# Kernel optimization log

Measured on AMD Instinct MI355X. Metric: run time of the kernel, lower is better.

## Reference

```python
import jax, jax.numpy as jnp
import numpy as np

B, R, C, H, W = 4, 2, 19, 256, 512


def setup_inputs() -> dict:
    key = jax.random.key(0)
    k1, k2, k3 = jax.random.split(key, 3)
    return {
        "ref_pred": jax.random.normal(k1, (B, R, C, H, W), dtype=jnp.float32),
        # motion vectors in quarter-pel units (divided by 4 inside forward);
        # scale so displacements span a few pixels
        "ref_mv": jax.random.normal(k2, (B, R, 2, H, W), dtype=jnp.float32) * 8.0,
        "ref_weight": jax.random.uniform(k3, (B, R, 1, H, W), dtype=jnp.float32),
    }


def _warp(img, mv):
    """Bilinear backward warp (grid_sample, zeros padding).
    img: [N, C, H, W], mv: [N, 2, H, W] pixel displacements (x, y)."""
    N, Ch, Hh, Ww = img.shape
    ys, xs = jnp.meshgrid(jnp.arange(Hh, dtype=mv.dtype),
                          jnp.arange(Ww, dtype=mv.dtype), indexing="ij")
    gx = xs + mv[:, 0]  # [N, H, W] sample x-coordinate
    gy = ys + mv[:, 1]  # [N, H, W] sample y-coordinate
    x0 = jnp.floor(gx); y0 = jnp.floor(gy)
    x1 = x0 + 1.0;      y1 = y0 + 1.0
    wx1 = gx - x0; wx0 = 1.0 - wx1
    wy1 = gy - y0; wy0 = 1.0 - wy1

    img_flat = img.reshape(N, Ch, Hh * Ww)

    def samp(iy, ix):
        valid = ((ix >= 0) & (ix <= Ww - 1) & (iy >= 0) & (iy <= Hh - 1))
        iyc = jnp.clip(iy, 0, Hh - 1).astype(jnp.int32)
        ixc = jnp.clip(ix, 0, Ww - 1).astype(jnp.int32)
        lin = (iyc * Ww + ixc).reshape(N, 1, Hh * Ww)
        vals = jnp.take_along_axis(
            img_flat, jnp.broadcast_to(lin, (N, Ch, Hh * Ww)), axis=2
        ).reshape(N, Ch, Hh, Ww)
        return vals * valid.astype(img.dtype)[:, None]

    out = (samp(y0, x0) * (wy0 * wx0)[:, None]
           + samp(y0, x1) * (wy0 * wx1)[:, None]
           + samp(y1, x0) * (wy1 * wx0)[:, None]
           + samp(y1, x1) * (wy1 * wx1)[:, None])
    return out


def reference(ref_pred, ref_mv, ref_weight):
    Bb, Rr = ref_pred.shape[:2]
    pred = ref_pred.reshape(Bb * Rr, *ref_pred.shape[2:])   # [B*R, C, H, W]
    mv = ref_mv.reshape(Bb * Rr, *ref_mv.shape[2:]) / 4.0    # quarter-pel -> pixel
    # eval mode, eval_noise_sigma=0 -> no noise added
    warped = _warp(pred, mv)                                  # [B*R, C, H, W]
    w = ref_weight.reshape(Bb * Rr, *ref_weight.shape[2:])   # [B*R, 1, H, W]
    warped = warped * w
    return warped.reshape(Bb, Rr, *warped.shape[1:]).sum(axis=1)  # [B, C, H, W]
```

## Files before the change

### kernel.cpp

```cpp
#include <hip/hip_runtime.h>

constexpr int B = 4, R = 2, C = 19, H = 256, W = 512;
constexpr int HW = H * W;

constexpr int BX = 64, BY = 16;
constexpr int NBX = W / BX;
constexpr int NBY = H / BY;
constexpr int NSPAT = B * NBX * NBY;

constexpr int TW = 92;
constexpr int TH = 42;
constexpr int TILE_N = TW * TH;
constexpr int TILE_V4 = TILE_N / 4;

__global__ __launch_bounds__(256, 4) void mc_warp_kernel(
    const float* __restrict__ pred,
    const float* __restrict__ mv,
    const float* __restrict__ wgt,
    float* __restrict__ out)
{
    __shared__ float tile0[TILE_N];
    __shared__ float tile1[TILE_N];

    int t = threadIdx.x;
    int xcd  = blockIdx.x & 7;
    int slot = blockIdx.x >> 3;
    int vblk = xcd * (NSPAT / 8) + slot;
    int bx   = vblk & (NBX - 1);
    int by   = (vblk >> 3) & (NBY - 1);
    int b    = vblk >> 7;
    int x0 = bx * BX, y0 = by * BY;
    int tx = t & 15, ty = t >> 4;
    int y  = y0 + ty;
    int xb = x0 + tx * 4;

    int rowbase = min(max(y0 - 12, 0), H - TH);
    int colbase = min(max(x0 - 12, 0), W - TW);

    int   off0[R][4], off1[R][4];
    int   offL0[R][4], offL1[R][4], offG0[R][4], offG1[R][4];
    float wq[R][4][4];
    int flag = 0;

    #pragma unroll
    for (int r = 0; r < R; ++r) {
        const float* mvp = mv + (size_t)((b * R + r) * 2) * HW + (size_t)y * W + xb;
        float4 mx4 = *(const float4*)(mvp);
        float4 my4 = *(const float4*)(mvp + HW);
        float4 wr4 = *(const float4*)(wgt + (size_t)(b * R + r) * HW + (size_t)y * W + xb);
        float mxs[4] = {mx4.x, mx4.y, mx4.z, mx4.w};
        float mys[4] = {my4.x, my4.y, my4.z, my4.w};
        float wrs[4] = {wr4.x, wr4.y, wr4.z, wr4.w};
        #pragma unroll
        for (int p = 0; p < 4; ++p) {
            int x = xb + p;
            float gx = (float)x + mxs[p] * 0.25f;
            float gy = (float)y + mys[p] * 0.25f;
            float fx0 = floorf(gx), fy0 = floorf(gy);
            float wx1 = gx - fx0, wx0 = 1.0f - wx1;
            float wy1 = gy - fy0, wy0 = 1.0f - wy1;
            int ix0 = (int)fx0, iy0 = (int)fy0;
            int ix1 = ix0 + 1,  iy1 = iy0 + 1;

            int base = min(max(ix0, 0), W - 2);
            float wA = (ix0 == base)     ? wx0 : ((ix1 == base)     ? wx1 : 0.0f);
            float wB = (ix1 == base + 1) ? wx1 : ((ix0 == base + 1) ? wx0 : 0.0f);
            float wr = wrs[p];
            float wy0v = ((iy0 >= 0) && (iy0 < H)) ? wy0 * wr : 0.0f;
            float wy1v = ((iy1 >= 0) && (iy1 < H)) ? wy1 * wr : 0.0f;
            int cy0 = min(max(iy0, 0), H - 1);
            int cy1 = min(max(iy1, 0), H - 1);

            int l0 = base - colbase;
            int r0 = cy0 - rowbase, r1 = cy1 - rowbase;
            bool anyx = (wA != 0.0f) || (wB != 0.0f);
            bool anyy = (wy0v != 0.0f) || (wy1v != 0.0f);
            bool cb  = (l0 < 0 || l0 > TW - 2) && anyx && anyy;
            bool rb0 = (r0 < 0 || r0 > TH - 1) && (wy0v != 0.0f) && anyx;
            bool rb1 = (r1 < 0 || r1 > TH - 1) && (wy1v != 0.0f) && anyx;
            flag |= (int)(cb || rb0 || rb1);
            l0 = min(max(l0, 0), TW - 2);
            r0 = min(max(r0, 0), TH - 1);
            r1 = min(max(r1, 0), TH - 1);

            offL0[r][p] = r0 * TW + l0;
            offL1[r][p] = r1 * TW + l0;
            offG0[r][p] = cy0 * W + base;
            offG1[r][p] = cy1 * W + base;
            wq[r][p][0] = wy0v * wA;
            wq[r][p][1] = wy0v * wB;
            wq[r][p][2] = wy1v * wA;
            wq[r][p][3] = wy1v * wB;
        }
    }

    int fbB = __syncthreads_or(flag);
    #pragma unroll
    for (int r = 0; r < R; ++r)
        #pragma unroll
        for (int p = 0; p < 4; ++p) {
            off0[r][p] = fbB ? offG0[r][p] : offL0[r][p];
            off1[r][p] = fbB ? offG1[r][p] : offL1[r][p];
        }

    const float* pl0 = pred + (size_t)(b * R + 0) * C * HW;
    const float* pl1 = pred + (size_t)(b * R + 1) * C * HW;
    const float* st0 = pl0 + (size_t)rowbase * W + colbase;
    const float* st1 = pl1 + (size_t)rowbase * W + colbase;
    float* ob = out + (size_t)b * C * HW + (size_t)y * W + xb;

    int cbeg = (blockIdx.y == 0) ? 0 : 10;
    int cend = (blockIdx.y == 0) ? 10 : 19;

    for (int c = cbeg; c < cend; ++c) {
        if (c > cbeg) __syncthreads();
        if (!fbB) {
            const float* s0 = st0 + (size_t)c * HW;
            const float* s1 = st1 + (size_t)c * HW;
            #pragma unroll
            for (int i = 0; i < 4; ++i) {
                int idx = t + i * 256;
                if (idx < TILE_V4) {
                    int row = idx / 23;
                    int c4  = (idx - row * 23) * 4;
                    float4 v0 = *(const float4*)(s0 + row * W + c4);
                    float4 v1 = *(const float4*)(s1 + row * W + c4);
                    *(float4*)&tile0[row * TW + c4] = v0;
                    *(float4*)&tile1[row * TW + c4] = v1;
                }
            }
        }
        __syncthreads();

        float res[4];
        if (!fbB) {
            #pragma unroll
            for (int p = 0; p < 4; ++p) {
                float a00 = tile0[off0[0][p]], a01 = tile0[off0[0][p] + 1];
                float a10 = tile0[off1[0][p]], a11 = tile0[off1[0][p] + 1];
                float b00 = tile1[off0[1][p]], b01 = tile1[off0[1][p] + 1];
                float b10 = tile1[off1[1][p]], b11 = tile1[off1[1][p] + 1];
                res[p] = wq[0][p][0] * a00 + wq[0][p][1] * a01
                       + wq[0][p][2] * a10 + wq[0][p][3] * a11
                       + wq[1][p][0] * b00 + wq[1][p][1] * b01
                       + wq[1][p][2] * b10 + wq[1][p][3] * b11;
            }
        } else {
            const float* pc0 = pl0 + (size_t)c * HW;
            const float* pc1 = pl1 + (size_t)c * HW;
            #pragma unroll
            for (int p = 0; p < 4; ++p) {
                float a00 = pc0[off0[0][p]], a01 = pc0[off0[0][p] + 1];
                float a10 = pc0[off1[0][p]], a11 = pc0[off1[0][p] + 1];
                float b00 = pc1[off0[1][p]], b01 = pc1[off0[1][p] + 1];
                float b10 = pc1[off1[1][p]], b11 = pc1[off1[1][p] + 1];
                res[p] = wq[0][p][0] * a00 + wq[0][p][1] * a01
                       + wq[0][p][2] * a10 + wq[0][p][3] * a11
                       + wq[1][p][0] * b00 + wq[1][p][1] * b01
                       + wq[1][p][2] * b10 + wq[1][p][3] * b11;
            }
        }
        *(float4*)(ob + (size_t)c * HW) = make_float4(res[0], res[1], res[2], res[3]);
    }
}

extern "C" void kernel_launch(void* const* d_in, const int* in_sizes, int n_in,
                              void* d_out, int out_size, void* d_ws, size_t ws_size,
                              hipStream_t stream) {
    const float* pred = (const float*)d_in[0];
    const float* mv   = (const float*)d_in[1];
    const float* wgt  = (const float*)d_in[2];
    float* out = (float*)d_out;

    dim3 grid(NSPAT, 2);
    mc_warp_kernel<<<grid, dim3(256), 0, stream>>>(pred, mv, wgt, out);
}
```

Before: 153.8 us.

## Double-buffer channel tiles with async global-to-LDS loads and smaller halo

Replaces the synchronous per-channel global-to-register-to-LDS tile copy with `global_load_lds` direct copies into a double-buffered LDS tile. The next channel is prefetched while the current one is interpolated, so load latency overlaps compute and one barrier per channel is dropped. The halo tile shrinks from 92x42 to 88x38, reducing bytes loaded per channel. The cost is twice the LDS per block (launch bounds lowered to 3 blocks) and a higher chance that a block's motion vectors leave the tile and fall back to the slow direct-global path.

```diff
diff --git a/kernel.cpp b/kernel.cpp
--- a/kernel.cpp
+++ b/kernel.cpp
@@ -8,19 +8,25 @@
 constexpr int NBY = H / BY;
 constexpr int NSPAT = B * NBX * NBY;
 
-constexpr int TW = 92;
-constexpr int TH = 42;
+constexpr int TW = 88;
+constexpr int TH = 38;
 constexpr int TILE_N = TW * TH;
 constexpr int TILE_V4 = TILE_N / 4;
-
-__global__ __launch_bounds__(256, 4) void mc_warp_kernel(
+constexpr int ROW_V4 = TW / 4;
+
+__device__ __forceinline__ void dma16(const float* g, float* l) {
+    __builtin_amdgcn_global_load_lds(
+        (const __attribute__((address_space(1))) void*)g,
+        (__attribute__((address_space(3))) void*)l, 16, 0, 0);
+}
+
+__global__ __launch_bounds__(256, 3) void mc_warp_kernel(
     const float* __restrict__ pred,
     const float* __restrict__ mv,
     const float* __restrict__ wgt,
     float* __restrict__ out)
 {
-    __shared__ float tile0[TILE_N];
-    __shared__ float tile1[TILE_N];
+    __shared__ float tiles[2][2][TILE_N];
 
     int t = threadIdx.x;
     int xcd  = blockIdx.x & 7;
@@ -34,7 +40,7 @@
     int y  = y0 + ty;
     int xb = x0 + tx * 4;
 
-    int rowbase = min(max(y0 - 12, 0), H - TH);
+    int rowbase = min(max(y0 - 11, 0), H - TH);
     int colbase = min(max(x0 - 12, 0), W - TW);
 
     int   off0[R][4], off1[R][4];
@@ -103,6 +109,17 @@
             off1[r][p] = fbB ? offG1[r][p] : offL1[r][p];
         }
 
+    int sgoff[4], smask[4], ldsoff[4];
+    #pragma unroll
+    for (int i = 0; i < 4; ++i) {
+        int idx = t + 256 * i;
+        smask[i]  = idx < TILE_V4;
+        int row = idx / ROW_V4;
+        int col = (idx - row * ROW_V4) * 4;
+        sgoff[i]  = row * W + col;
+        ldsoff[i] = 4 * idx;
+    }
+
     const float* pl0 = pred + (size_t)(b * R + 0) * C * HW;
     const float* pl1 = pred + (size_t)(b * R + 1) * C * HW;
     const float* st0 = pl0 + (size_t)rowbase * W + colbase;
@@ -112,39 +129,45 @@
     int cbeg = (blockIdx.y == 0) ? 0 : 10;
     int cend = (blockIdx.y == 0) ? 10 : 19;
 
+    if (!fbB) {
+        const float* s0 = st0 + (size_t)cbeg * HW;
+        const float* s1 = st1 + (size_t)cbeg * HW;
+        #pragma unroll
+        for (int i = 0; i < 4; ++i) if (smask[i]) {
+            dma16(s0 + sgoff[i], &tiles[0][0][ldsoff[i]]);
+            dma16(s1 + sgoff[i], &tiles[0][1][ldsoff[i]]);
+        }
+    }
+
+    int cur = 0;
     for (int c = cbeg; c < cend; ++c) {
-        if (c > cbeg) __syncthreads();
+        float res[4];
         if (!fbB) {
-            const float* s0 = st0 + (size_t)c * HW;
-            const float* s1 = st1 + (size_t)c * HW;
-            #pragma unroll
-            for (int i = 0; i < 4; ++i) {
-                int idx = t + i * 256;
-                if (idx < TILE_V4) {
-                    int row = idx / 23;
-                    int c4  = (idx - row * 23) * 4;
-                    float4 v0 = *(const float4*)(s0 + row * W + c4);
-                    float4 v1 = *(const float4*)(s1 + row * W + c4);
-                    *(float4*)&tile0[row * TW + c4] = v0;
-                    *(float4*)&tile1[row * TW + c4] = v1;
+            __syncthreads();
+            if (c + 1 < cend) {
+                const float* s0 = st0 + (size_t)(c + 1) * HW;
+                const float* s1 = st1 + (size_t)(c + 1) * HW;
+                int nb = cur ^ 1;
+                #pragma unroll
+                for (int i = 0; i < 4; ++i) if (smask[i]) {
+                    dma16(s0 + sgoff[i], &tiles[nb][0][ldsoff[i]]);
+                    dma16(s1 + sgoff[i], &tiles[nb][1][ldsoff[i]]);
                 }
             }
-        }
-        __syncthreads();
-
-        float res[4];
-        if (!fbB) {
+            const float* t0 = tiles[cur][0];
+            const float* t1 = tiles[cur][1];
             #pragma unroll
             for (int p = 0; p < 4; ++p) {
-                float a00 = tile0[off0[0][p]], a01 = tile0[off0[0][p] + 1];
-                float a10 = tile0[off1[0][p]], a11 = tile0[off1[0][p] + 1];
-                float b00 = tile1[off0[1][p]], b01 = tile1[off0[1][p] + 1];
-                float b10 = tile1[off1[1][p]], b11 = tile1[off1[1][p] + 1];
+                float a00 = t0[off0[0][p]], a01 = t0[off0[0][p] + 1];
+                float a10 = t0[off1[0][p]], a11 = t0[off1[0][p] + 1];
+                float b00 = t1[off0[1][p]], b01 = t1[off0[1][p] + 1];
+                float b10 = t1[off1[1][p]], b11 = t1[off1[1][p] + 1];
                 res[p] = wq[0][p][0] * a00 + wq[0][p][1] * a01
                        + wq[0][p][2] * a10 + wq[0][p][3] * a11
                        + wq[1][p][0] * b00 + wq[1][p][1] * b01
                        + wq[1][p][2] * b10 + wq[1][p][3] * b11;
             }
+            cur ^= 1;
         } else {
             const float* pc0 = pl0 + (size_t)c * HW;
             const float* pc1 = pl1 + (size_t)c * HW;
```

Result: slower. 158.9 us (+3.3%).
